# Performance work log

Measured on AMD Instinct MI355X. Metric: run time of the kernel, lower is better.

The kernel has to match this reference:

```python
import jax, jax.numpy as jnp
import numpy as np

B, A, G = 256, 64, 978          # batch, n_atoms, num_gene
D_DRUG, D_CELL, D_DOSE = 128, 50, 128
CELL_IN, DOSE_IN = 978, 12
GLOBAL = D_DRUG + D_CELL + D_DOSE   # 306
EXP_IN = GLOBAL + 128               # 434
E, TOP_K = 4, 2


def setup_inputs() -> dict:
    key = jax.random.key(0)
    ks = jax.random.split(key, 24)
    w = lambda k, s: jax.random.normal(k, s, jnp.float32) * 0.05
    return {
        "drug_atom_embed": jax.random.normal(ks[0], (B, A, D_DRUG), jnp.float32),
        "input_cell_gex": jax.random.normal(ks[1], (B, CELL_IN), jnp.float32),
        "input_pert_idose": jax.random.normal(ks[2], (B, DOSE_IN), jnp.float32),
        # LinearEncoder: 978 -> 200 -> 100 -> 50 (ReLU after each)
        "cell_W1": w(ks[3], (CELL_IN, 200)), "cell_b1": jnp.zeros((200,), jnp.float32),
        "cell_W2": w(ks[4], (200, 100)),     "cell_b2": jnp.zeros((100,), jnp.float32),
        "cell_W3": w(ks[5], (100, D_CELL)),  "cell_b3": jnp.zeros((D_CELL,), jnp.float32),
        # DoseEncoder: 12 -> 64 -> 128 (ReLU after each; dropout off at eval)
        "dose_W1": w(ks[6], (DOSE_IN, 64)),  "dose_b1": jnp.zeros((64,), jnp.float32),
        "dose_W2": w(ks[7], (64, D_DOSE)),   "dose_b2": jnp.zeros((D_DOSE,), jnp.float32),
        # gene index embedding [num_gene, 128]
        "gene_emb": w(ks[8], (G, 128)),
        # GatingNetwork: 306 -> 128 -> 4
        "gate_W1": w(ks[9], (GLOBAL, 128)),  "gate_b1": jnp.zeros((128,), jnp.float32),
        "gate_W2": w(ks[10], (128, E)),      "gate_b2": jnp.zeros((E,), jnp.float32),
        # 4 ExpertNetworks stacked: 434 -> 128 -> 1
        "exp_W1": w(ks[11], (E, EXP_IN, 128)), "exp_b1": jnp.zeros((E, 128), jnp.float32),
        "exp_W2": w(ks[12], (E, 128, 1)),      "exp_b2": jnp.zeros((E, 1), jnp.float32),
    }


def reference(drug_atom_embed, input_cell_gex, input_pert_idose,
              cell_W1, cell_b1, cell_W2, cell_b2, cell_W3, cell_b3,
              dose_W1, dose_b1, dose_W2, dose_b2, gene_emb,
              gate_W1, gate_b1, gate_W2, gate_b2,
              exp_W1, exp_b1, exp_W2, exp_b2):
    relu = jax.nn.relu
    # drug: sum atom embeddings -> [B, 128]
    drug = drug_atom_embed.sum(axis=1)
    # cell encoder -> [B, 50]
    cell = relu(input_cell_gex @ cell_W1 + cell_b1)
    cell = relu(cell @ cell_W2 + cell_b2)
    cell = relu(cell @ cell_W3 + cell_b3)
    # dose encoder -> [B, 128]
    dose = relu(input_pert_idose @ dose_W1 + dose_b1)
    dose = relu(dose @ dose_W2 + dose_b2)
    # global features [B, 306]
    g = jnp.concatenate([drug, cell, dose], axis=1)
    # gating: top-k sparse gates [B, E]
    logits = relu(g @ gate_W1 + gate_b1) @ gate_W2 + gate_b2
    top_v, top_i = jax.lax.top_k(logits, TOP_K)
    top_g = jax.nn.softmax(top_v, axis=1)
    gates = jnp.zeros_like(logits).at[jnp.arange(logits.shape[0])[:, None], top_i].set(top_g)
    # gene-aware expert input [B, G, 434]
    expert_input = jnp.concatenate([
        jnp.broadcast_to(g[:, None, :], (g.shape[0], G, GLOBAL)),
        jnp.broadcast_to(gene_emb[None, :, :], (g.shape[0], G, 128)),
    ], axis=2)
    # all experts: [B, E, G, 128] -> [B, E, G]
    h = relu(jnp.einsum('bgi,eih->begh', expert_input, exp_W1) + exp_b1[None, :, None, :])
    o = jnp.einsum('begh,eho->beg', h, exp_W2) + exp_b2[None, :, :1]  # exp_b2[e,0] broadcast
    predictions = jnp.einsum('beg,be->bg', o, gates)
    return predictions, cell
```

## Files before the change

kernel.cpp:

```cpp
#include <hip/hip_runtime.h>

#define NB 256
#define NA 64
#define NG 978
#define CELL_IN 978
#define DOSE_IN 12
#define GLOBAL_F 306
#define EXP_IN 434
#define NE 4

#define WS_SEL 0
#define WS_U   (WS_SEL + NB*4)
#define WS_V   (WS_U + NB*256)

#define AB_GRID (NB + 245)

__device__ __forceinline__ float wave_reduce(float p) {
    #pragma unroll
    for (int off = 32; off > 0; off >>= 1) p += __shfl_down(p, off, 64);
    return p;
}

__global__ __launch_bounds__(1024) void ab_kernel(
    const float* __restrict__ drug, const float* __restrict__ gex,
    const float* __restrict__ idose,
    const float* __restrict__ cW1, const float* __restrict__ cb1,
    const float* __restrict__ cW2, const float* __restrict__ cb2,
    const float* __restrict__ cW3, const float* __restrict__ cb3,
    const float* __restrict__ dW1, const float* __restrict__ db1,
    const float* __restrict__ dW2, const float* __restrict__ db2,
    const float* __restrict__ gW1, const float* __restrict__ gb1,
    const float* __restrict__ gW2, const float* __restrict__ gb2,
    const float* __restrict__ eW1, const float* __restrict__ eb1,
    const float* __restrict__ gene,
    float* __restrict__ ws, float* __restrict__ cell_out)
{
    __shared__ float s_gex[CELL_IN];
    __shared__ float s_g[GLOBAL_F];
    __shared__ float s_h1[200];
    __shared__ float s_h2[100];
    __shared__ float s_gh[128];
    __shared__ float s_d1[64];
    __shared__ int   s_isel[2];
    __shared__ float s_part[16 * 200];
    __shared__ float s_pu[32 * 128];
    __shared__ float s_ag[4][128];
    __shared__ float s_ap[4][8][128];

    const int blk = blockIdx.x, tid = threadIdx.x;

    if (blk >= NB) {
        const int gq = tid >> 8, lt = tid & 255;
        const int g = (blk - NB) * 4 + gq;
        if (lt < 128) s_ag[gq][lt] = (g < NG) ? gene[g * 128 + lt] : 0.f;
        __syncthreads();
        const int e = lt >> 6, ks = (lt >> 5) & 1, h4 = lt & 31;
        const float* wp = eW1 + ((size_t)e * EXP_IN + GLOBAL_F) * 128 + 4 * h4;
        float4 acc = {0.f, 0.f, 0.f, 0.f};
        const int k0 = ks * 64;
        #pragma unroll 8
        for (int k = k0; k < k0 + 64; ++k) {
            float4 w = *(const float4*)(wp + (size_t)k * 128);
            float x = s_ag[gq][k];
            acc.x += x * w.x; acc.y += x * w.y; acc.z += x * w.z; acc.w += x * w.w;
        }
        *(float4*)(&s_ap[gq][e * 2 + ks][4 * h4]) = acc;
        __syncthreads();
        if (lt < 128 && g < NG) {
            int oe = lt >> 5, oh4 = lt & 31;
            float4 p0 = *(const float4*)(&s_ap[gq][oe * 2 + 0][4 * oh4]);
            float4 p1 = *(const float4*)(&s_ap[gq][oe * 2 + 1][4 * oh4]);
            float4 o = {p0.x + p1.x, p0.y + p1.y, p0.z + p1.z, p0.w + p1.w};
            *(float4*)(ws + WS_V + (size_t)g * 512 + oe * 128 + 4 * oh4) = o;
        }
        return;
    }

    const int b = blk;

    if (tid < CELL_IN) s_gex[tid] = gex[b * CELL_IN + tid];
    {
        int row = tid >> 7, d = tid & 127;
        const float* p = drug + ((size_t)b * NA) * 128 + d;
        float acc = 0.f;
        #pragma unroll
        for (int i = 0; i < 8; ++i) acc += p[(size_t)(i * 8 + row) * 128];
        s_pu[row * 128 + d] = acc;
    }
    __syncthreads();
    if (tid < 128) {
        float a = 0.f;
        #pragma unroll
        for (int r = 0; r < 8; ++r) a += s_pu[r * 128 + tid];
        s_g[tid] = a;
    } else if (tid < 192) {
        int j = tid - 128;
        float acc = db1[j];
        #pragma unroll
        for (int i = 0; i < DOSE_IN; ++i)
            acc += idose[b * DOSE_IN + i] * dW1[i * 64 + j];
        s_d1[j] = fmaxf(acc, 0.f);
    }
    __syncthreads();
    if (tid < 128) {
        float acc = db2[tid];
        #pragma unroll 8
        for (int i = 0; i < 64; ++i) acc += s_d1[i] * dW2[i * 128 + tid];
        s_g[178 + tid] = fmaxf(acc, 0.f);
    }
    __syncthreads();

    {
        int q = tid & 63, ks = tid >> 6;
        if (q < 50) {
            int i0 = ks * 62, i1 = min(i0 + 62, CELL_IN);
            float4 acc = {0.f, 0.f, 0.f, 0.f};
            #pragma unroll 4
            for (int i = i0; i < i1; ++i) {
                float4 w = *(const float4*)(cW1 + (size_t)i * 200 + 4 * q);
                float x = s_gex[i];
                acc.x += x * w.x; acc.y += x * w.y; acc.z += x * w.z; acc.w += x * w.w;
            }
            *(float4*)(&s_part[ks * 200 + 4 * q]) = acc;
        }
    }
    __syncthreads();
    if (tid < 200) {
        float a = cb1[tid];
        #pragma unroll
        for (int ks = 0; ks < 16; ++ks) a += s_part[ks * 200 + tid];
        s_h1[tid] = fmaxf(a, 0.f);
    }
    __syncthreads();

    {
        int q = tid & 31, ks = tid >> 5;
        if (q < 25 && ks < 16) {
            int i0 = ks * 13, i1 = min(i0 + 13, 200);
            float4 acc = {0.f, 0.f, 0.f, 0.f};
            #pragma unroll
            for (int i = i0; i < i1; ++i) {
                float4 w = *(const float4*)(cW2 + (size_t)i * 100 + 4 * q);
                float x = s_h1[i];
                acc.x += x * w.x; acc.y += x * w.y; acc.z += x * w.z; acc.w += x * w.w;
            }
            *(float4*)(&s_part[ks * 100 + 4 * q]) = acc;
        }
    }
    __syncthreads();
    if (tid < 100) {
        float a = cb2[tid];
        #pragma unroll
        for (int ks = 0; ks < 16; ++ks) a += s_part[ks * 100 + tid];
        s_h2[tid] = fmaxf(a, 0.f);
    }
    __syncthreads();

    {
        int j = tid & 63, ks = tid >> 6;
        if (j < 50 && ks < 8) {
            int i0 = ks * 13, i1 = min(i0 + 13, 100);
            float acc = 0.f;
            #pragma unroll
            for (int i = i0; i < i1; ++i) acc += s_h2[i] * cW3[i * 50 + j];
            s_part[ks * 64 + j] = acc;
        }
    }
    __syncthreads();
    if (tid < 50) {
        float a = cb3[tid];
        #pragma unroll
        for (int ks = 0; ks < 8; ++ks) a += s_part[ks * 64 + tid];
        float r = fmaxf(a, 0.f);
        s_g[128 + tid] = r;
        cell_out[b * 50 + tid] = r;
    }
    __syncthreads();

    {
        int q = tid & 31, ks = tid >> 5;
        if (ks < 16) {
            int i0 = ks * 20, i1 = min(i0 + 20, GLOBAL_F);
            float4 acc = {0.f, 0.f, 0.f, 0.f};
            #pragma unroll
            for (int i = i0; i < i1; ++i) {
                float4 w = *(const float4*)(gW1 + (size_t)i * 128 + 4 * q);
                float x = s_g[i];
                acc.x += x * w.x; acc.y += x * w.y; acc.z += x * w.z; acc.w += x * w.w;
            }
            *(float4*)(&s_part[ks * 128 + 4 * q]) = acc;
        }
    }
    __syncthreads();
    if (tid < 128) {
        float a = gb1[tid];
        #pragma unroll
        for (int ks = 0; ks < 16; ++ks) a += s_part[ks * 128 + tid];
        s_gh[tid] = fmaxf(a, 0.f);
    }
    __syncthreads();

    if (tid < 64) {
        float h0 = s_gh[tid], h1 = s_gh[tid + 64];
        float logit[NE];
        #pragma unroll
        for (int j = 0; j < NE; ++j) {
            float p = h0 * gW2[tid * NE + j] + h1 * gW2[(tid + 64) * NE + j];
            p = wave_reduce(p);
            logit[j] = p + gb2[j];
        }
        if (tid == 0) {
            int i1 = 0; float v1 = logit[0];
            #pragma unroll
            for (int i = 1; i < NE; ++i) if (logit[i] > v1) { v1 = logit[i]; i1 = i; }
            int i2 = -1; float v2 = -__builtin_inff();
            #pragma unroll
            for (int i = 0; i < NE; ++i) {
                if (i == i1) continue;
                if (logit[i] > v2) { v2 = logit[i]; i2 = i; }
            }
            float ex = __expf(v2 - v1);
            float inv = 1.f / (1.f + ex);
            s_isel[0] = i1; s_isel[1] = i2;
            ws[WS_SEL + b * 4 + 0] = (float)i1;
            ws[WS_SEL + b * 4 + 1] = (float)i2;
            ws[WS_SEL + b * 4 + 2] = inv;
            ws[WS_SEL + b * 4 + 3] = ex * inv;
        }
    }
    __syncthreads();

    {
        int es = tid >> 9, ks = (tid >> 5) & 15, h4 = tid & 31;
        int e = s_isel[es];
        int i0 = ks * 20, i1 = min(i0 + 20, GLOBAL_F);
        const float* wp = eW1 + (size_t)e * EXP_IN * 128 + 4 * h4;
        float4 acc = {0.f, 0.f, 0.f, 0.f};
        #pragma unroll
        for (int i = i0; i < i1; ++i) {
            float4 w = *(const float4*)(wp + (size_t)i * 128);
            float x = s_g[i];
            acc.x += x * w.x; acc.y += x * w.y; acc.z += x * w.z; acc.w += x * w.w;
        }
        *(float4*)(&s_pu[(es * 16 + ks) * 128 + 4 * h4]) = acc;
    }
    __syncthreads();
    if (tid < 256) {
        int es = tid >> 7, h = tid & 127;
        int e = s_isel[es];
        float a = eb1[e * 128 + h];
        #pragma unroll
        for (int ks = 0; ks < 16; ++ks) a += s_pu[(es * 16 + ks) * 128 + h];
        ws[WS_U + (size_t)b * 256 + es * 128 + h] = a;
    }
}

#define GT 28
#define BT 16
__global__ __launch_bounds__(256) void c_kernel(
    const float* __restrict__ eW2, const float* __restrict__ eb2,
    const float* __restrict__ ws, float* __restrict__ pred)
{
    __shared__ float s_v[GT * 520];
    __shared__ float s_u[BT * 260];
    __shared__ float s_w2[512];
    __shared__ float s_sel[BT * 4];
    const int bt = blockIdx.x & 15, gt = blockIdx.x >> 4, tid = threadIdx.x;
    const int b0 = bt * BT, g0 = gt * GT;

    if (tid < BT * 4) s_sel[tid] = ws[WS_SEL + b0 * 4 + tid];
    for (int i = tid; i < 512; i += 256) s_w2[i] = eW2[i];
    for (int i4 = tid; i4 < BT * 64; i4 += 256) {
        int bl = i4 >> 6, h4 = i4 & 63;
        float4 u = *(const float4*)(ws + WS_U + (size_t)(b0 + bl) * 256 + 4 * h4);
        *(float4*)(&s_u[bl * 260 + 4 * h4]) = u;
    }
    for (int i4 = tid; i4 < GT * 128; i4 += 256) {
        int gl = i4 >> 7, h4 = i4 & 127;
        int g = g0 + gl;
        float4 v = {0.f, 0.f, 0.f, 0.f};
        if (g < NG) v = *(const float4*)(ws + WS_V + (size_t)g * 512 + 4 * h4);
        *(float4*)(&s_v[gl * 520 + 4 * h4]) = v;
    }
    __syncthreads();

    const int bl = tid & 15;
    const int ea = (int)s_sel[bl * 4 + 0], eb = (int)s_sel[bl * 4 + 1];
    const float gA = s_sel[bl * 4 + 2], gB = s_sel[bl * 4 + 3];
    const float bA = eb2[ea], bB = eb2[eb];
    #pragma unroll
    for (int it = 0; it < 2; ++it) {
        int gl = (tid >> 4) + 16 * it;
        int g = g0 + gl;
        if (gl < GT && g < NG) {
            const float* vA = s_v + gl * 520 + ea * 128;
            const float* vB = s_v + gl * 520 + eb * 128;
            const float* uA = s_u + bl * 260;
            const float* uB = uA + 128;
            const float* wA = s_w2 + ea * 128;
            const float* wB = s_w2 + eb * 128;
            float dA = 0.f, dB = 0.f;
            #pragma unroll 8
            for (int k = 0; k < 32; ++k) {
                float4 va = *(const float4*)(vA + 4 * k);
                float4 ua = *(const float4*)(uA + 4 * k);
                float4 wa = *(const float4*)(wA + 4 * k);
                dA += fmaxf(ua.x + va.x, 0.f) * wa.x + fmaxf(ua.y + va.y, 0.f) * wa.y
                    + fmaxf(ua.z + va.z, 0.f) * wa.z + fmaxf(ua.w + va.w, 0.f) * wa.w;
                float4 vb = *(const float4*)(vB + 4 * k);
                float4 ub = *(const float4*)(uB + 4 * k);
                float4 wb = *(const float4*)(wB + 4 * k);
                dB += fmaxf(ub.x + vb.x, 0.f) * wb.x + fmaxf(ub.y + vb.y, 0.f) * wb.y
                    + fmaxf(ub.z + vb.z, 0.f) * wb.z + fmaxf(ub.w + vb.w, 0.f) * wb.w;
            }
            pred[(size_t)(b0 + bl) * NG + g] = gA * (dA + bA) + gB * (dB + bB);
        }
    }
}

extern "C" void kernel_launch(void* const* d_in, const int* in_sizes, int n_in,
                              void* d_out, int out_size, void* d_ws, size_t ws_size,
                              hipStream_t stream) {
    const float* drug  = (const float*)d_in[0];
    const float* gex   = (const float*)d_in[1];
    const float* idose = (const float*)d_in[2];
    const float* cW1 = (const float*)d_in[3];  const float* cb1 = (const float*)d_in[4];
    const float* cW2 = (const float*)d_in[5];  const float* cb2 = (const float*)d_in[6];
    const float* cW3 = (const float*)d_in[7];  const float* cb3 = (const float*)d_in[8];
    const float* dW1 = (const float*)d_in[9];  const float* db1 = (const float*)d_in[10];
    const float* dW2 = (const float*)d_in[11]; const float* db2 = (const float*)d_in[12];
    const float* gene = (const float*)d_in[13];
    const float* gW1 = (const float*)d_in[14]; const float* gb1 = (const float*)d_in[15];
    const float* gW2 = (const float*)d_in[16]; const float* gb2 = (const float*)d_in[17];
    const float* eW1 = (const float*)d_in[18]; const float* eb1 = (const float*)d_in[19];
    const float* eW2 = (const float*)d_in[20]; const float* eb2 = (const float*)d_in[21];

    float* ws   = (float*)d_ws;
    float* out  = (float*)d_out;
    float* pred = out;
    float* cell = out + NB * NG;

    ab_kernel<<<AB_GRID, 1024, 0, stream>>>(drug, gex, idose,
        cW1, cb1, cW2, cb2, cW3, cb3, dW1, db1, dW2, db2,
        gW1, gb1, gW2, gb2, eW1, eb1, gene, ws, cell);
    c_kernel<<<16 * 35, 256, 0, stream>>>(eW2, eb2, ws, pred);
}
```

Baseline: 167.3 us.

## Restructure expert output kernel to one batch row per block with direct V reads

The c_kernel stops tiling 16 batches by 28 genes with V staged in shared memory. Each block now handles one batch row and a quarter of the genes. Each thread reads its gene's V rows for the two selected experts straight from global memory (L2-resident), while u and W2 sit in shared memory as broadcast values. This removes the large shared-memory staging and raises the grid to 1024 blocks. The cost is that V is re-read once per batch row, which adds global/L2 traffic in place of shared-memory reuse across batches.

```diff
diff --git a/kernel.cpp b/kernel.cpp
--- a/kernel.cpp
+++ b/kernel.cpp
@@ -255,66 +255,42 @@
     }
 }
 
-#define GT 28
-#define BT 16
 __global__ __launch_bounds__(256) void c_kernel(
     const float* __restrict__ eW2, const float* __restrict__ eb2,
     const float* __restrict__ ws, float* __restrict__ pred)
 {
-    __shared__ float s_v[GT * 520];
-    __shared__ float s_u[BT * 260];
-    __shared__ float s_w2[512];
-    __shared__ float s_sel[BT * 4];
-    const int bt = blockIdx.x & 15, gt = blockIdx.x >> 4, tid = threadIdx.x;
-    const int b0 = bt * BT, g0 = gt * GT;
-
-    if (tid < BT * 4) s_sel[tid] = ws[WS_SEL + b0 * 4 + tid];
-    for (int i = tid; i < 512; i += 256) s_w2[i] = eW2[i];
-    for (int i4 = tid; i4 < BT * 64; i4 += 256) {
-        int bl = i4 >> 6, h4 = i4 & 63;
-        float4 u = *(const float4*)(ws + WS_U + (size_t)(b0 + bl) * 256 + 4 * h4);
-        *(float4*)(&s_u[bl * 260 + 4 * h4]) = u;
-    }
-    for (int i4 = tid; i4 < GT * 128; i4 += 256) {
-        int gl = i4 >> 7, h4 = i4 & 127;
-        int g = g0 + gl;
-        float4 v = {0.f, 0.f, 0.f, 0.f};
-        if (g < NG) v = *(const float4*)(ws + WS_V + (size_t)g * 512 + 4 * h4);
-        *(float4*)(&s_v[gl * 520 + 4 * h4]) = v;
-    }
-    __syncthreads();
-
-    const int bl = tid & 15;
-    const int ea = (int)s_sel[bl * 4 + 0], eb = (int)s_sel[bl * 4 + 1];
-    const float gA = s_sel[bl * 4 + 2], gB = s_sel[bl * 4 + 3];
+    __shared__ float s_u[256];
+    __shared__ float s_w2[256];
+    const int b = blockIdx.x >> 2, qt = blockIdx.x & 3, tid = threadIdx.x;
+
+    const int ea = (int)ws[WS_SEL + b * 4 + 0];
+    const int eb = (int)ws[WS_SEL + b * 4 + 1];
+    const float gA = ws[WS_SEL + b * 4 + 2];
+    const float gB = ws[WS_SEL + b * 4 + 3];
     const float bA = eb2[ea], bB = eb2[eb];
-    #pragma unroll
-    for (int it = 0; it < 2; ++it) {
-        int gl = (tid >> 4) + 16 * it;
-        int g = g0 + gl;
-        if (gl < GT && g < NG) {
-            const float* vA = s_v + gl * 520 + ea * 128;
-            const float* vB = s_v + gl * 520 + eb * 128;
-            const float* uA = s_u + bl * 260;
-            const float* uB = uA + 128;
-            const float* wA = s_w2 + ea * 128;
-            const float* wB = s_w2 + eb * 128;
-            float dA = 0.f, dB = 0.f;
-            #pragma unroll 8
-            for (int k = 0; k < 32; ++k) {
-                float4 va = *(const float4*)(vA + 4 * k);
-                float4 ua = *(const float4*)(uA + 4 * k);
-                float4 wa = *(const float4*)(wA + 4 * k);
-                dA += fmaxf(ua.x + va.x, 0.f) * wa.x + fmaxf(ua.y + va.y, 0.f) * wa.y
-                    + fmaxf(ua.z + va.z, 0.f) * wa.z + fmaxf(ua.w + va.w, 0.f) * wa.w;
-                float4 vb = *(const float4*)(vB + 4 * k);
-                float4 ub = *(const float4*)(uB + 4 * k);
-                float4 wb = *(const float4*)(wB + 4 * k);
-                dB += fmaxf(ub.x + vb.x, 0.f) * wb.x + fmaxf(ub.y + vb.y, 0.f) * wb.y
-                    + fmaxf(ub.z + vb.z, 0.f) * wb.z + fmaxf(ub.w + vb.w, 0.f) * wb.w;
-            }
-            pred[(size_t)(b0 + bl) * NG + g] = gA * (dA + bA) + gB * (dB + bB);
-        }
+
+    s_u[tid] = ws[WS_U + (size_t)b * 256 + tid];
+    s_w2[tid] = (tid < 128) ? eW2[ea * 128 + tid] : eW2[eb * 128 + (tid - 128)];
+    __syncthreads();
+
+    const int g = qt * 256 + tid;
+    if (g < NG) {
+        const float4* vA = (const float4*)(ws + WS_V + (size_t)g * 512 + ea * 128);
+        const float4* vB = (const float4*)(ws + WS_V + (size_t)g * 512 + eb * 128);
+        float dA = 0.f, dB = 0.f;
+        #pragma unroll 8
+        for (int k = 0; k < 32; ++k) {
+            float4 va = vA[k], vb = vB[k];
+            dA += fmaxf(s_u[4*k+0] + va.x, 0.f) * s_w2[4*k+0]
+                + fmaxf(s_u[4*k+1] + va.y, 0.f) * s_w2[4*k+1]
+                + fmaxf(s_u[4*k+2] + va.z, 0.f) * s_w2[4*k+2]
+                + fmaxf(s_u[4*k+3] + va.w, 0.f) * s_w2[4*k+3];
+            dB += fmaxf(s_u[128+4*k+0] + vb.x, 0.f) * s_w2[128+4*k+0]
+                + fmaxf(s_u[128+4*k+1] + vb.y, 0.f) * s_w2[128+4*k+1]
+                + fmaxf(s_u[128+4*k+2] + vb.z, 0.f) * s_w2[128+4*k+2]
+                + fmaxf(s_u[128+4*k+3] + vb.w, 0.f) * s_w2[128+4*k+3];
+        }
+        pred[(size_t)b * NG + g] = gA * (dA + bA) + gB * (dB + bB);
     }
 }
 
@@ -343,5 +319,5 @@
     ab_kernel<<<AB_GRID, 1024, 0, stream>>>(drug, gex, idose,
         cW1, cb1, cW2, cb2, cW3, cb3, dW1, db1, dW2, db2,
         gW1, gb1, gW2, gb2, eW1, eb1, gene, ws, cell);
-    c_kernel<<<16 * 35, 256, 0, stream>>>(eW2, eb2, ws, pred);
+    c_kernel<<<NB * 4, 256, 0, stream>>>(eW2, eb2, ws, pred);
 }
```

New measurement: 184.2 us. 10.1% more time.
